# Optimization experiments

Hardware: AMD Instinct MI355X
Metric: run time of the kernel (lower is better)

Reference implementation:

```python
import jax, jax.numpy as jnp
import numpy as np

B, S, H = 16, 2048, 1024

def setup_inputs() -> dict:
    key = jax.random.key(0)
    ks = jax.random.split(key, 6)
    return {
        "h": jax.random.normal(ks[0], (1, B, H), jnp.float32),
        "c": jax.random.normal(ks[1], (1, B, H), jnp.float32),
        "encoder_outputs": jax.random.normal(ks[2], (B, S, H), jnp.float32),
        "attn_W": jax.random.normal(ks[3], (H, 2 * H), jnp.float32) * 0.02,
        "attn_b": jax.random.normal(ks[4], (H,), jnp.float32) * 0.02,
        "v_W": jax.random.normal(ks[5], (1, H), jnp.float32) * 0.02,
    }

def reference(h, c, encoder_outputs, attn_W, attn_b, v_W):
    # h: (1,B,H) -> (B,1,H); a: (B,S,H)
    a = encoder_outputs
    hq = jnp.transpose(h, (1, 0, 2))  # (B,1,H)
    # cat((s, a), -1) @ attn_W.T == s @ Wh.T + a @ Wa.T (avoids (B,S,2H) buffer)
    Wh, Wa = attn_W[:, :H], attn_W[:, H:]
    energy = jax.nn.relu(
        jnp.einsum("bqh,oh->bqo", hq, Wh)          # (B,1,H), broadcast over S
        + jnp.einsum("bsh,oh->bso", a, Wa)
        + attn_b
    )  # (B,S,H)
    scores = jnp.einsum("bsh,h->bs", energy, v_W[0])  # (B,S)
    attn_weights = jax.nn.softmax(scores, axis=1)      # (B,S)
    context = jnp.einsum("bs,bsh->bh", attn_weights, a)[:, None, :]  # (B,1,H)
    return context, attn_weights
```

## Files before the change

kernel.cpp:

```cpp
#include <hip/hip_runtime.h>
#include <hip/hip_bf16.h>


typedef __bf16 bf16x8 __attribute__((ext_vector_type(8)));
typedef float floatx4 __attribute__((ext_vector_type(4)));

#define BB 16
#define SS 2048
#define HH 1024
#define MM (BB * SS)

#define GLB(p) ((const __attribute__((address_space(1))) void*)(p))
#define LDSP(p) ((__attribute__((address_space(3))) void*)(p))

__device__ inline ushort f2bf(float x) {
    uint32_t u = __builtin_bit_cast(uint32_t, x);
    u += 0x7FFFu + ((u >> 16) & 1u);
    return (ushort)(u >> 16);
}

__global__ __launch_bounds__(256) void prep_all_kernel(
    const float* __restrict__ h, const float* __restrict__ W,
    const float* __restrict__ bias, const float* __restrict__ a,
    float* __restrict__ projh, __bf16* __restrict__ Wb, __bf16* __restrict__ Ab,
    float* __restrict__ sp0, float* __restrict__ ctx)
{
    int bid = blockIdx.x;
    int tid = threadIdx.x;
    if (bid >= 336) {
        size_t i = (size_t)(bid - 336) * 256 + tid;
        const float* s = a + i * 8;
        float4 x = *(const float4*)(s);
        float4 y = *(const float4*)(s + 4);
        union { ushort u[8]; uint4 v; } p;
        p.u[0] = f2bf(x.x); p.u[1] = f2bf(x.y); p.u[2] = f2bf(x.z); p.u[3] = f2bf(x.w);
        p.u[4] = f2bf(y.x); p.u[5] = f2bf(y.y); p.u[6] = f2bf(y.z); p.u[7] = f2bf(y.w);
        *(uint4*)(Ab + i * 8) = p.v;
    } else if (bid < 256) {
        int b = bid >> 4;
        int oc = bid & 15;
        __shared__ float hrow[HH];
        *(float4*)&hrow[tid * 4] = *(const float4*)(h + (size_t)b * HH + tid * 4);
        __syncthreads();
        int ol = tid >> 2;
        int kq = tid & 3;
        int o = oc * 64 + ol;
        const float* wr = W + (size_t)o * (2 * HH) + kq * 256;
        const float* hb = hrow + kq * 256;
        float sum = 0.f;
        for (int k = 0; k < 256; k += 4) {
            float4 wv = *(const float4*)(wr + k);
            sum += hb[k] * wv.x + hb[k + 1] * wv.y + hb[k + 2] * wv.z + hb[k + 3] * wv.w;
        }
        sum += __shfl_xor(sum, 1);
        sum += __shfl_xor(sum, 2);
        if (kq == 0) projh[b * HH + o] = sum + bias[o];
    } else if (bid < 320) {
        int cb = bid - 256;
#pragma unroll
        for (int j = 0; j < 8; j++) {
            int g = cb * 2048 + tid + j * 256;
            int o = g >> 7;
            int k = (g & 127) * 8;
            const float* s = W + (size_t)o * (2 * HH) + HH + k;
            float4 x = *(const float4*)(s);
            float4 y = *(const float4*)(s + 4);
            union { ushort u[8]; uint4 v; } p;
            p.u[0] = f2bf(x.x); p.u[1] = f2bf(x.y); p.u[2] = f2bf(x.z); p.u[3] = f2bf(x.w);
            p.u[4] = f2bf(y.x); p.u[5] = f2bf(y.y); p.u[6] = f2bf(y.z); p.u[7] = f2bf(y.w);
            *(uint4*)(Wb + (size_t)o * HH + k) = p.v;
        }
    } else {
        int zb = bid - 320;
        float4 z = make_float4(0.f, 0.f, 0.f, 0.f);
        float* sp = sp0 + zb * 2048 + tid * 8;
        *(float4*)(sp) = z;
        *(float4*)(sp + 4) = z;
        *(float4*)(ctx + zb * 1024 + tid * 4) = z;
    }
}

__global__ __launch_bounds__(512, 2) void gemm_scores_kernel(
    const __bf16* __restrict__ Ab,
    const __bf16* __restrict__ Wb,
    const float* __restrict__ projh,
    const float* __restrict__ vW,
    float* __restrict__ scores_part)
{
    __shared__ __bf16 smem[32768];

    const int bid = blockIdx.x;
    const int m0 = (((bid >> 5) << 3) + (bid & 7)) * 256;
    const int nq = (bid >> 3) & 3;
    const int n0 = nq * 256;
    const int bidx = m0 >> 11;

    const int tid = threadIdx.x;
    const int lane = tid & 63;
    const int wave = tid >> 6;
    const int wm = (wave & 1) * 128;
    const int wn = (wave >> 1) * 64;
    const int quad = lane >> 4;
    const int l16 = lane & 15;

    floatx4 acc[8][4];
    const floatx4 z = {0.f, 0.f, 0.f, 0.f};
#pragma unroll
    for (int i = 0; i < 8; i++)
#pragma unroll
        for (int j = 0; j < 4; j++) acc[i][j] = z;

    const int su = tid >> 3;
    const int sj = (tid & 7) ^ (su & 7);
    const int g_row = su * 2 + (sj >> 2);
    const int g_col = (sj & 3) * 8;
    const __bf16* gA  = Ab + (size_t)(m0 + g_row) * HH + g_col;
    const __bf16* gA2 = gA + (size_t)128 * HH;
    const __bf16* gB  = Wb + (size_t)(n0 + g_row) * HH + g_col;
    const __bf16* gB2 = gB + (size_t)128 * HH;
    const int ldsb = wave * 512;

    int aoff[8], boff[4];
#pragma unroll
    for (int i = 0; i < 8; i++) {
        int frow = wm + i * 16 + l16;
        int u2 = frow >> 1;
        int cc = u2 * 8 + (((((frow & 1) << 2) | quad)) ^ (u2 & 7));
        aoff[i] = cc * 8;
    }
#pragma unroll
    for (int j = 0; j < 4; j++) {
        int frow = wn + j * 16 + l16;
        int u2 = frow >> 1;
        int cc = u2 * 8 + (((((frow & 1) << 2) | quad)) ^ (u2 & 7));
        boff[j] = 8192 + cc * 8;
    }

#define ISSUE_STAGE(buf, k0)                                                          \
    {                                                                                 \
        __bf16* dst = smem + (buf) * 16384 + ldsb;                                    \
        __builtin_amdgcn_global_load_lds(GLB(gA  + (k0)), LDSP(dst),         16, 0, 0); \
        __builtin_amdgcn_global_load_lds(GLB(gA2 + (k0)), LDSP(dst + 4096),  16, 0, 0); \
        __builtin_amdgcn_global_load_lds(GLB(gB  + (k0)), LDSP(dst + 8192),  16, 0, 0); \
        __builtin_amdgcn_global_load_lds(GLB(gB2 + (k0)), LDSP(dst + 12288), 16, 0, 0); \
    }

    ISSUE_STAGE(0, 0)
    for (int s = 0; s < 32; s++) {
        __syncthreads();
        if (s < 31) ISSUE_STAGE((s + 1) & 1, (s + 1) * 32)
        const __bf16* sb = smem + (s & 1) * 16384;
        bf16x8 af[8], bfr[4];
#pragma unroll
        for (int j = 0; j < 4; j++) bfr[j] = *(const bf16x8*)(sb + boff[j]);
#pragma unroll
        for (int i = 0; i < 8; i++) af[i] = *(const bf16x8*)(sb + aoff[i]);
#pragma unroll
        for (int i = 0; i < 8; i++)
#pragma unroll
            for (int j = 0; j < 4; j++)
                acc[i][j] = __builtin_amdgcn_mfma_f32_16x16x32_bf16(af[i], bfr[j], acc[i][j], 0, 0, 0);
    }
#undef ISSUE_STAGE

    float ph[4], vv[4];
#pragma unroll
    for (int j = 0; j < 4; j++) {
        int ng = n0 + wn + j * 16 + l16;
        ph[j] = projh[bidx * HH + ng];
        vv[j] = vW[ng];
    }

    float* red = (float*)smem;
    if (tid < 256) red[tid] = 0.f;
    __syncthreads();

#pragma unroll
    for (int i = 0; i < 8; i++) {
        float s[4] = {0.f, 0.f, 0.f, 0.f};
#pragma unroll
        for (int j = 0; j < 4; j++) {
#pragma unroll
            for (int r2 = 0; r2 < 4; r2++) {
                float e = acc[i][j][r2] + ph[j];
                e = e > 0.f ? e : 0.f;
                s[r2] += e * vv[j];
            }
        }
#pragma unroll
        for (int r2 = 0; r2 < 4; r2++) {
            s[r2] += __shfl_xor(s[r2], 1);
            s[r2] += __shfl_xor(s[r2], 2);
            s[r2] += __shfl_xor(s[r2], 4);
            s[r2] += __shfl_xor(s[r2], 8);
        }
        if (l16 == 0) {
#pragma unroll
            for (int r2 = 0; r2 < 4; r2++)
                atomicAdd(&red[wm + i * 16 + quad * 4 + r2], s[r2]);
        }
    }
    __syncthreads();
    if (tid < 256) scores_part[(size_t)nq * MM + m0 + tid] = red[tid];
}

__global__ __launch_bounds__(256) void gemm_scores_f32_kernel(
    const float* __restrict__ A, const float* __restrict__ W,
    const float* __restrict__ projh, const float* __restrict__ vW,
    float* __restrict__ scores)
{
    constexpr int BM = 128, BN = 128, BK = 32, LDT = BK + 8;
    __shared__ __bf16 As[BM * LDT];
    __shared__ __bf16 Bs[BN * LDT];
    const int n0 = blockIdx.x * BN;
    const int m0 = blockIdx.y * BM;
    const int bidx = m0 >> 11;
    const int tid = threadIdx.x;
    const int lane = tid & 63;
    const int wave = tid >> 6;
    const int wm = (wave & 1) * 64;
    const int wn = (wave >> 1) * 64;
    const int quad = lane >> 4;
    const int l16 = lane & 15;
    floatx4 acc[4][4];
    const floatx4 z = {0.f, 0.f, 0.f, 0.f};
#pragma unroll
    for (int i = 0; i < 4; i++)
#pragma unroll
        for (int j = 0; j < 4; j++) acc[i][j] = z;
    int rowT[4], colT[4];
#pragma unroll
    for (int i = 0; i < 4; i++) {
        int fi = tid + 256 * i;
        rowT[i] = fi >> 3;
        colT[i] = (fi & 7) * 4;
    }
    for (int k0 = 0; k0 < HH; k0 += BK) {
        float4 av[4], bv[4];
#pragma unroll
        for (int i = 0; i < 4; i++) {
            av[i] = *(const float4*)(A + (size_t)(m0 + rowT[i]) * HH + k0 + colT[i]);
            bv[i] = *(const float4*)(W + (size_t)(n0 + rowT[i]) * (2 * HH) + HH + k0 + colT[i]);
        }
        __syncthreads();
#pragma unroll
        for (int i = 0; i < 4; i++) {
            ushort4 ua = make_ushort4(f2bf(av[i].x), f2bf(av[i].y), f2bf(av[i].z), f2bf(av[i].w));
            ushort4 ub = make_ushort4(f2bf(bv[i].x), f2bf(bv[i].y), f2bf(bv[i].z), f2bf(bv[i].w));
            *(ushort4*)&As[rowT[i] * LDT + colT[i]] = ua;
            *(ushort4*)&Bs[rowT[i] * LDT + colT[i]] = ub;
        }
        __syncthreads();
        bf16x8 af[4], bf[4];
#pragma unroll
        for (int i = 0; i < 4; i++)
            af[i] = *(const bf16x8*)&As[(wm + i * 16 + l16) * LDT + quad * 8];
#pragma unroll
        for (int j = 0; j < 4; j++)
            bf[j] = *(const bf16x8*)&Bs[(wn + j * 16 + l16) * LDT + quad * 8];
#pragma unroll
        for (int i = 0; i < 4; i++)
#pragma unroll
            for (int j = 0; j < 4; j++)
                acc[i][j] = __builtin_amdgcn_mfma_f32_16x16x32_bf16(af[i], bf[j], acc[i][j], 0, 0, 0);
    }
    float ph[4], vv[4];
#pragma unroll
    for (int j = 0; j < 4; j++) {
        int ng = n0 + wn + j * 16 + l16;
        ph[j] = projh[bidx * HH + ng];
        vv[j] = vW[ng];
    }
#pragma unroll
    for (int i = 0; i < 4; i++) {
        float s[4] = {0.f, 0.f, 0.f, 0.f};
#pragma unroll
        for (int j = 0; j < 4; j++) {
#pragma unroll
            for (int r = 0; r < 4; r++) {
                float e = acc[i][j][r] + ph[j];
                e = e > 0.f ? e : 0.f;
                s[r] += e * vv[j];
            }
        }
#pragma unroll
        for (int r = 0; r < 4; r++) {
            s[r] += __shfl_xor(s[r], 1);
            s[r] += __shfl_xor(s[r], 2);
            s[r] += __shfl_xor(s[r], 4);
            s[r] += __shfl_xor(s[r], 8);
        }
        if (l16 == 0) {
#pragma unroll
            for (int r = 0; r < 4; r++) {
                int mg = m0 + wm + i * 16 + quad * 4 + r;
                atomicAdd(&scores[mg], s[r]);
            }
        }
    }
}

__global__ __launch_bounds__(256) void softmax_context_kernel(
    const __bf16* __restrict__ Ab, const float* __restrict__ scores_part,
    int nparts, float* __restrict__ wout, float* __restrict__ ctx)
{
    int b = blockIdx.x >> 5;
    int sc = blockIdx.x & 31;
    int tid = threadIdx.x;
    const float* srow = scores_part + b * SS;

    float x[8];
    float mx = -1e30f;
#pragma unroll
    for (int i = 0; i < 8; i++) {
        int idx = tid + i * 256;
        float v = srow[idx];
        for (int q = 1; q < nparts; q++) v += srow[(size_t)q * MM + idx];
        x[i] = v; mx = fmaxf(mx, v);
    }
#pragma unroll
    for (int off = 32; off; off >>= 1) mx = fmaxf(mx, __shfl_xor(mx, off));
    __shared__ float redm[4], reds[4];
    if ((tid & 63) == 0) redm[tid >> 6] = mx;
    __syncthreads();
    mx = fmaxf(fmaxf(redm[0], redm[1]), fmaxf(redm[2], redm[3]));
    float sum = 0.f;
#pragma unroll
    for (int i = 0; i < 8; i++) sum += __expf(x[i] - mx);
#pragma unroll
    for (int off = 32; off; off >>= 1) sum += __shfl_xor(sum, off);
    if ((tid & 63) == 0) reds[tid >> 6] = sum;
    __syncthreads();
    float inv = 1.0f / (reds[0] + reds[1] + reds[2] + reds[3]);

    __shared__ float wsm[64];
    if (tid < 64) {
        int idx = sc * 64 + tid;
        float v = srow[idx];
        for (int q = 1; q < nparts; q++) v += srow[(size_t)q * MM + idx];
        float wv = __expf(v - mx) * inv;
        wsm[tid] = wv;
        wout[b * SS + idx] = wv;
    }
    __syncthreads();

    const __bf16* arow = Ab + ((size_t)b * SS + sc * 64) * HH + tid * 4;
    float4 acc = make_float4(0.f, 0.f, 0.f, 0.f);
#pragma unroll 4
    for (int s = 0; s < 64; s++) {
        float w = wsm[s];
        uint2 uv = *(const uint2*)(arow + (size_t)s * HH);
        float a0 = __builtin_bit_cast(float, uv.x << 16);
        float a1 = __builtin_bit_cast(float, uv.x & 0xffff0000u);
        float a2 = __builtin_bit_cast(float, uv.y << 16);
        float a3 = __builtin_bit_cast(float, uv.y & 0xffff0000u);
        acc.x += w * a0; acc.y += w * a1; acc.z += w * a2; acc.w += w * a3;
    }
    float* o = ctx + b * HH + tid * 4;
    atomicAdd(o + 0, acc.x);
    atomicAdd(o + 1, acc.y);
    atomicAdd(o + 2, acc.z);
    atomicAdd(o + 3, acc.w);
}

__global__ __launch_bounds__(256) void softmax_context_f32_kernel(
    const float* __restrict__ A, const float* __restrict__ scores_part,
    float* __restrict__ wout, float* __restrict__ ctx)
{
    int b = blockIdx.x >> 5;
    int sc = blockIdx.x & 31;
    int tid = threadIdx.x;
    const float* srow = scores_part + b * SS;
    float x[8];
    float mx = -1e30f;
#pragma unroll
    for (int i = 0; i < 8; i++) { x[i] = srow[tid + i * 256]; mx = fmaxf(mx, x[i]); }
#pragma unroll
    for (int off = 32; off; off >>= 1) mx = fmaxf(mx, __shfl_xor(mx, off));
    __shared__ float redm[4], reds[4];
    if ((tid & 63) == 0) redm[tid >> 6] = mx;
    __syncthreads();
    mx = fmaxf(fmaxf(redm[0], redm[1]), fmaxf(redm[2], redm[3]));
    float sum = 0.f;
#pragma unroll
    for (int i = 0; i < 8; i++) sum += __expf(x[i] - mx);
#pragma unroll
    for (int off = 32; off; off >>= 1) sum += __shfl_xor(sum, off);
    if ((tid & 63) == 0) reds[tid >> 6] = sum;
    __syncthreads();
    float inv = 1.0f / (reds[0] + reds[1] + reds[2] + reds[3]);
    __shared__ float wsm[64];
    if (tid < 64) {
        float wv = __expf(srow[sc * 64 + tid] - mx) * inv;
        wsm[tid] = wv;
        wout[b * SS + sc * 64 + tid] = wv;
    }
    __syncthreads();
    const float* arow = A + ((size_t)b * SS + sc * 64) * HH + tid * 4;
    float4 acc = make_float4(0.f, 0.f, 0.f, 0.f);
#pragma unroll 4
    for (int s = 0; s < 64; s++) {
        float w = wsm[s];
        float4 v = *(const float4*)(arow + (size_t)s * HH);
        acc.x += w * v.x; acc.y += w * v.y; acc.z += w * v.z; acc.w += w * v.w;
    }
    float* o = ctx + b * HH + tid * 4;
    atomicAdd(o + 0, acc.x);
    atomicAdd(o + 1, acc.y);
    atomicAdd(o + 2, acc.z);
    atomicAdd(o + 3, acc.w);
}

extern "C" void kernel_launch(void* const* d_in, const int* in_sizes, int n_in,
                              void* d_out, int out_size, void* d_ws, size_t ws_size,
                              hipStream_t stream) {
    const float* h    = (const float*)d_in[0];
    const float* a    = (const float*)d_in[2];
    const float* W    = (const float*)d_in[3];
    const float* bias = (const float*)d_in[4];
    const float* vW   = (const float*)d_in[5];
    float* out = (float*)d_out;

    float* projh       = (float*)d_ws;
    float* scores_part = projh + BB * HH;
    __bf16* Wb = (__bf16*)(scores_part + 4 * MM);
    __bf16* Ab = Wb + (size_t)HH * HH;
    const size_t need = (size_t)(BB * HH + 4 * MM) * 4 + (size_t)HH * HH * 2
                      + (size_t)MM * HH * 2;

    if (ws_size >= need) {
        prep_all_kernel<<<336 + MM * HH / 8 / 256, 256, 0, stream>>>(
            h, W, bias, a, projh, Wb, Ab, scores_part, out);
        gemm_scores_kernel<<<512, 512, 0, stream>>>(Ab, Wb, projh, vW, scores_part);
        softmax_context_kernel<<<BB * 32, 256, 0, stream>>>(
            Ab, scores_part, 4, out + BB * HH, out);
    } else {
        prep_all_kernel<<<336, 256, 0, stream>>>(h, W, bias, a, projh, Wb, Ab, scores_part, out);
        gemm_scores_f32_kernel<<<dim3(HH / 128, MM / 128), 256, 0, stream>>>(
            a, W, projh, vW, scores_part);
        softmax_context_f32_kernel<<<BB * 32, 256, 0, stream>>>(
            a, scores_part, out + BB * HH, out);
    }
}
```

Before: 299.1 us.

## Deepen GEMM LDS pipeline to four stages with split A/B loads and setprio

Replaces the double-buffered k-loop in the scores GEMM with a 4-slot LDS ring (64K bf16 of shared memory). A and B halves are staged separately and interleaved with half-tile MFMA phases, using explicit vmcnt/lgkmcnt waits, raw barriers and s_setprio around MFMA bursts. The goal is to hide global-to-LDS load latency behind more compute than the one-stage-ahead prefetch allowed. The cost is doubled LDS per block (128 KB), which may prevent the two-blocks-per-CU occupancy hinted by launch bounds. The hand-tuned wait counts and tail loads that wrap to k=0 also risk subtle synchronisation errors.

Result: faster. 292.3 us (-2.3%).

```diff
diff --git a/kernel.cpp b/kernel.cpp
--- a/kernel.cpp
+++ b/kernel.cpp
@@ -87,7 +87,7 @@
     const float* __restrict__ vW,
     float* __restrict__ scores_part)
 {
-    __shared__ __bf16 smem[32768];
+    __shared__ __bf16 smem[65536];
 
     const int bid = blockIdx.x;
     const int m0 = (((bid >> 5) << 3) + (bid & 7)) * 256;
@@ -114,54 +114,132 @@
     const int sj = (tid & 7) ^ (su & 7);
     const int g_row = su * 2 + (sj >> 2);
     const int g_col = (sj & 3) * 8;
-    const __bf16* gA  = Ab + (size_t)(m0 + g_row) * HH + g_col;
-    const __bf16* gA2 = gA + (size_t)128 * HH;
-    const __bf16* gB  = Wb + (size_t)(n0 + g_row) * HH + g_col;
-    const __bf16* gB2 = gB + (size_t)128 * HH;
-    const int ldsb = wave * 512;
+    const __bf16* gA0 = Ab + (size_t)(m0 + g_row) * HH + g_col;
+    const __bf16* gA1 = gA0 + (size_t)128 * HH;
+    const __bf16* gB0 = Wb + (size_t)(n0 + g_row) * HH + g_col;
+    const __bf16* gB1 = gB0 + (size_t)128 * HH;
+    const int wchunk = wave * 512;
 
     int aoff[8], boff[4];
 #pragma unroll
     for (int i = 0; i < 8; i++) {
         int frow = wm + i * 16 + l16;
-        int u2 = frow >> 1;
-        int cc = u2 * 8 + (((((frow & 1) << 2) | quad)) ^ (u2 & 7));
-        aoff[i] = cc * 8;
+        int r7 = frow & 127;
+        int u2 = r7 >> 1;
+        int cc = u2 * 8 + (((((r7 & 1) << 2) | quad)) ^ (u2 & 7));
+        aoff[i] = (frow >> 7) * 4096 + cc * 8;
     }
 #pragma unroll
     for (int j = 0; j < 4; j++) {
         int frow = wn + j * 16 + l16;
-        int u2 = frow >> 1;
-        int cc = u2 * 8 + (((((frow & 1) << 2) | quad)) ^ (u2 & 7));
-        boff[j] = 8192 + cc * 8;
-    }
-
-#define ISSUE_STAGE(buf, k0)                                                          \
-    {                                                                                 \
-        __bf16* dst = smem + (buf) * 16384 + ldsb;                                    \
-        __builtin_amdgcn_global_load_lds(GLB(gA  + (k0)), LDSP(dst),         16, 0, 0); \
-        __builtin_amdgcn_global_load_lds(GLB(gA2 + (k0)), LDSP(dst + 4096),  16, 0, 0); \
-        __builtin_amdgcn_global_load_lds(GLB(gB  + (k0)), LDSP(dst + 8192),  16, 0, 0); \
-        __builtin_amdgcn_global_load_lds(GLB(gB2 + (k0)), LDSP(dst + 12288), 16, 0, 0); \
-    }
-
-    ISSUE_STAGE(0, 0)
-    for (int s = 0; s < 32; s++) {
-        __syncthreads();
-        if (s < 31) ISSUE_STAGE((s + 1) & 1, (s + 1) * 32)
-        const __bf16* sb = smem + (s & 1) * 16384;
-        bf16x8 af[8], bfr[4];
-#pragma unroll
-        for (int j = 0; j < 4; j++) bfr[j] = *(const bf16x8*)(sb + boff[j]);
-#pragma unroll
-        for (int i = 0; i < 8; i++) af[i] = *(const bf16x8*)(sb + aoff[i]);
-#pragma unroll
-        for (int i = 0; i < 8; i++)
-#pragma unroll
-            for (int j = 0; j < 4; j++)
-                acc[i][j] = __builtin_amdgcn_mfma_f32_16x16x32_bf16(af[i], bfr[j], acc[i][j], 0, 0, 0);
-    }
-#undef ISSUE_STAGE
+        int r7 = frow & 127;
+        int u2 = r7 >> 1;
+        int cc = u2 * 8 + (((((r7 & 1) << 2) | quad)) ^ (u2 & 7));
+        boff[j] = 32768 + (frow >> 7) * 4096 + cc * 8;
+    }
+
+#define STAGE_A(slot, koff)                                                             \
+    {                                                                                   \
+        __bf16* d_ = smem + (slot) * 8192 + wchunk;                                     \
+        __builtin_amdgcn_global_load_lds(GLB(gA0 + (koff)), LDSP(d_), 16, 0, 0);        \
+        __builtin_amdgcn_global_load_lds(GLB(gA1 + (koff)), LDSP(d_ + 4096), 16, 0, 0); \
+    }
+#define STAGE_B(slot, koff)                                                             \
+    {                                                                                   \
+        __bf16* d_ = smem + 32768 + (slot) * 8192 + wchunk;                             \
+        __builtin_amdgcn_global_load_lds(GLB(gB0 + (koff)), LDSP(d_), 16, 0, 0);        \
+        __builtin_amdgcn_global_load_lds(GLB(gB1 + (koff)), LDSP(d_ + 4096), 16, 0, 0); \
+    }
+#define READ_BFR(base)                                     \
+    {                                                      \
+        bfr[0] = *(const bf16x8*)((base) + boff[0]);       \
+        bfr[1] = *(const bf16x8*)((base) + boff[1]);       \
+        bfr[2] = *(const bf16x8*)((base) + boff[2]);       \
+        bfr[3] = *(const bf16x8*)((base) + boff[3]);       \
+    }
+#define READ_ALO(base)                                     \
+    {                                                      \
+        af[0] = *(const bf16x8*)((base) + aoff[0]);        \
+        af[1] = *(const bf16x8*)((base) + aoff[1]);        \
+        af[2] = *(const bf16x8*)((base) + aoff[2]);        \
+        af[3] = *(const bf16x8*)((base) + aoff[3]);        \
+    }
+#define READ_AHI(base)                                     \
+    {                                                      \
+        af2[0] = *(const bf16x8*)((base) + aoff[4]);       \
+        af2[1] = *(const bf16x8*)((base) + aoff[5]);       \
+        af2[2] = *(const bf16x8*)((base) + aoff[6]);       \
+        af2[3] = *(const bf16x8*)((base) + aoff[7]);       \
+    }
+#define MFMA_LO                                                                            \
+    _Pragma("unroll") for (int i_ = 0; i_ < 4; i_++)                                       \
+        _Pragma("unroll") for (int j_ = 0; j_ < 4; j_++)                                   \
+            acc[i_][j_] = __builtin_amdgcn_mfma_f32_16x16x32_bf16(af[i_], bfr[j_], acc[i_][j_], 0, 0, 0);
+#define MFMA_HI                                                                            \
+    _Pragma("unroll") for (int i_ = 0; i_ < 4; i_++)                                       \
+        _Pragma("unroll") for (int j_ = 0; j_ < 4; j_++)                                   \
+            acc[i_ + 4][j_] = __builtin_amdgcn_mfma_f32_16x16x32_bf16(af2[i_], bfr[j_], acc[i_ + 4][j_], 0, 0, 0);
+#define BAR __builtin_amdgcn_s_barrier()
+#define LGKM0 asm volatile("s_waitcnt lgkmcnt(0)" ::: "memory")
+#define VM8 asm volatile("s_waitcnt vmcnt(8)" ::: "memory")
+#define PRIO1 __builtin_amdgcn_s_setprio(1)
+#define PRIO0 __builtin_amdgcn_s_setprio(0)
+
+#define SPAN(P, K1, K2)                              \
+    {                                                \
+        const __bf16* cb0 = smem + (P) * 16384;      \
+        const __bf16* cb1 = cb0 + 8192;              \
+                                        \
+        READ_BFR(cb0); READ_ALO(cb0);                \
+        STAGE_A((1 - (P)) * 2 + 1, K1);              \
+        BAR; LGKM0; PRIO1; MFMA_LO; PRIO0; BAR;      \
+                                        \
+        READ_AHI(cb0);                               \
+        STAGE_B((1 - (P)) * 2 + 1, K1);              \
+        VM8;                                         \
+        BAR; LGKM0; PRIO1; MFMA_HI; PRIO0; BAR;      \
+                                        \
+        READ_BFR(cb1); READ_ALO(cb1);                \
+        STAGE_A((P) * 2, K2);                        \
+        BAR; LGKM0; PRIO1; MFMA_LO; PRIO0; BAR;      \
+                                        \
+        READ_AHI(cb1);                               \
+        STAGE_B((P) * 2, K2);                        \
+        VM8;                                         \
+        BAR; LGKM0; PRIO1; MFMA_HI; PRIO0; BAR;      \
+    }
+
+    bf16x8 af[4], af2[4], bfr[4];
+
+    STAGE_A(0, 0);  STAGE_B(0, 0);
+    STAGE_A(1, 32); STAGE_B(1, 32);
+    STAGE_A(2, 64); STAGE_B(2, 64);
+    VM8;
+    BAR;
+
+    for (int it = 0; it < 8; ++it) {
+        const int kb = it * 128;
+        const int k1 = kb + 96;
+        const int k2 = (it < 7) ? kb + 128 : 0;
+        const int k3 = (it < 7) ? kb + 160 : 0;
+        const int k4 = (it < 7) ? kb + 192 : 0;
+        SPAN(0, k1, k2)
+        SPAN(1, k3, k4)
+    }
+
+#undef SPAN
+#undef STAGE_A
+#undef STAGE_B
+#undef READ_BFR
+#undef READ_ALO
+#undef READ_AHI
+#undef MFMA_LO
+#undef MFMA_HI
+#undef BAR
+#undef LGKM0
+#undef VM8
+#undef PRIO1
+#undef PRIO0
 
     float ph[4], vv[4];
 #pragma unroll
```

## Fuse fp32-to-bf16 conversion of encoder outputs into GEMM LDS pipeline

Applied to the files above, without the earlier changes.

Drops the separate pass that converted encoder outputs to bf16. The GEMM kernel now streams fp32 A tiles into LDS with a triple-buffered async pipeline and converts them to bf16 in registers before the MFMAs, with barriers, waitcnts and priority hints. The context kernel reads fp32 encoder outputs directly. This removes a full-tensor read/write pass, but the GEMM and context reads double in bytes and the larger LDS footprint lowers occupancy.

After: 288.0 us. -3.7%, faster.

```diff
diff --git a/kernel.cpp b/kernel.cpp
--- a/kernel.cpp
+++ b/kernel.cpp
@@ -21,22 +21,13 @@
 
 __global__ __launch_bounds__(256) void prep_all_kernel(
     const float* __restrict__ h, const float* __restrict__ W,
-    const float* __restrict__ bias, const float* __restrict__ a,
-    float* __restrict__ projh, __bf16* __restrict__ Wb, __bf16* __restrict__ Ab,
+    const float* __restrict__ bias,
+    float* __restrict__ projh, __bf16* __restrict__ Wb,
     float* __restrict__ sp0, float* __restrict__ ctx)
 {
     int bid = blockIdx.x;
     int tid = threadIdx.x;
-    if (bid >= 336) {
-        size_t i = (size_t)(bid - 336) * 256 + tid;
-        const float* s = a + i * 8;
-        float4 x = *(const float4*)(s);
-        float4 y = *(const float4*)(s + 4);
-        union { ushort u[8]; uint4 v; } p;
-        p.u[0] = f2bf(x.x); p.u[1] = f2bf(x.y); p.u[2] = f2bf(x.z); p.u[3] = f2bf(x.w);
-        p.u[4] = f2bf(y.x); p.u[5] = f2bf(y.y); p.u[6] = f2bf(y.z); p.u[7] = f2bf(y.w);
-        *(uint4*)(Ab + i * 8) = p.v;
-    } else if (bid < 256) {
+    if (bid < 256) {
         int b = bid >> 4;
         int oc = bid & 15;
         __shared__ float hrow[HH];
@@ -81,13 +72,14 @@
 }
 
 __global__ __launch_bounds__(512, 2) void gemm_scores_kernel(
-    const __bf16* __restrict__ Ab,
+    const float* __restrict__ Af,
     const __bf16* __restrict__ Wb,
     const float* __restrict__ projh,
     const float* __restrict__ vW,
     float* __restrict__ scores_part)
 {
-    __shared__ __bf16 smem[32768];
+    __shared__ __align__(16) char smem_raw[147456];
+    __bf16* sB = (__bf16*)(smem_raw + 98304);
 
     const int bid = blockIdx.x;
     const int m0 = (((bid >> 5) << 3) + (bid & 7)) * 256;
@@ -110,58 +102,143 @@
 #pragma unroll
         for (int j = 0; j < 4; j++) acc[i][j] = z;
 
+    const int rb = lane >> 3;
+    const int cchunk = ((lane & 7) ^ rb) * 4;
+    const float* gAq0 = Af + (size_t)(m0 +   0 + wave * 8 + rb) * HH + cchunk;
+    const float* gAq1 = Af + (size_t)(m0 +  64 + wave * 8 + rb) * HH + cchunk;
+    const float* gAq2 = Af + (size_t)(m0 + 128 + wave * 8 + rb) * HH + cchunk;
+    const float* gAq3 = Af + (size_t)(m0 + 192 + wave * 8 + rb) * HH + cchunk;
+
     const int su = tid >> 3;
     const int sj = (tid & 7) ^ (su & 7);
     const int g_row = su * 2 + (sj >> 2);
     const int g_col = (sj & 3) * 8;
-    const __bf16* gA  = Ab + (size_t)(m0 + g_row) * HH + g_col;
-    const __bf16* gA2 = gA + (size_t)128 * HH;
-    const __bf16* gB  = Wb + (size_t)(n0 + g_row) * HH + g_col;
-    const __bf16* gB2 = gB + (size_t)128 * HH;
-    const int ldsb = wave * 512;
-
-    int aoff[8], boff[4];
-#pragma unroll
-    for (int i = 0; i < 8; i++) {
-        int frow = wm + i * 16 + l16;
-        int u2 = frow >> 1;
-        int cc = u2 * 8 + (((((frow & 1) << 2) | quad)) ^ (u2 & 7));
-        aoff[i] = cc * 8;
-    }
+    const __bf16* gB0 = Wb + (size_t)(n0 + g_row) * HH + g_col;
+    const __bf16* gB1 = gB0 + (size_t)128 * HH;
+
+    const int axL = (quad * 32) ^ ((l16 & 7) << 4);
+    const int axH = axL ^ 16;
+    int arow[8];
+#pragma unroll
+    for (int i = 0; i < 8; i++) arow[i] = (wm + i * 16 + l16) * 128;
+
+    int boff[4];
 #pragma unroll
     for (int j = 0; j < 4; j++) {
         int frow = wn + j * 16 + l16;
-        int u2 = frow >> 1;
-        int cc = u2 * 8 + (((((frow & 1) << 2) | quad)) ^ (u2 & 7));
-        boff[j] = 8192 + cc * 8;
-    }
-
-#define ISSUE_STAGE(buf, k0)                                                          \
-    {                                                                                 \
-        __bf16* dst = smem + (buf) * 16384 + ldsb;                                    \
-        __builtin_amdgcn_global_load_lds(GLB(gA  + (k0)), LDSP(dst),         16, 0, 0); \
-        __builtin_amdgcn_global_load_lds(GLB(gA2 + (k0)), LDSP(dst + 4096),  16, 0, 0); \
-        __builtin_amdgcn_global_load_lds(GLB(gB  + (k0)), LDSP(dst + 8192),  16, 0, 0); \
-        __builtin_amdgcn_global_load_lds(GLB(gB2 + (k0)), LDSP(dst + 12288), 16, 0, 0); \
-    }
-
-    ISSUE_STAGE(0, 0)
-    for (int s = 0; s < 32; s++) {
-        __syncthreads();
-        if (s < 31) ISSUE_STAGE((s + 1) & 1, (s + 1) * 32)
-        const __bf16* sb = smem + (s & 1) * 16384;
-        bf16x8 af[8], bfr[4];
-#pragma unroll
-        for (int j = 0; j < 4; j++) bfr[j] = *(const bf16x8*)(sb + boff[j]);
-#pragma unroll
-        for (int i = 0; i < 8; i++) af[i] = *(const bf16x8*)(sb + aoff[i]);
-#pragma unroll
-        for (int i = 0; i < 8; i++)
-#pragma unroll
-            for (int j = 0; j < 4; j++)
-                acc[i][j] = __builtin_amdgcn_mfma_f32_16x16x32_bf16(af[i], bfr[j], acc[i][j], 0, 0, 0);
-    }
-#undef ISSUE_STAGE
+        int r7 = frow & 127;
+        int u2 = r7 >> 1;
+        int cc = u2 * 8 + (((((r7 & 1) << 2) | quad)) ^ (u2 & 7));
+        boff[j] = (frow >> 7) * 4096 + cc * 8;
+    }
+
+#define STAGE_A(S, KF)                                                                       \
+    {                                                                                        \
+        char* dA_ = smem_raw + (S) * 32768 + wave * 1024;                                    \
+        __builtin_amdgcn_global_load_lds(GLB(gAq0 + (KF)), LDSP(dA_), 16, 0, 0);             \
+        __builtin_amdgcn_global_load_lds(GLB(gAq1 + (KF)), LDSP(dA_ + 8192), 16, 0, 0);      \
+        __builtin_amdgcn_global_load_lds(GLB(gAq2 + (KF)), LDSP(dA_ + 16384), 16, 0, 0);     \
+        __builtin_amdgcn_global_load_lds(GLB(gAq3 + (KF)), LDSP(dA_ + 24576), 16, 0, 0);     \
+    }
+#define STAGE_B(S, KF)                                                                       \
+    {                                                                                        \
+        __bf16* dB_ = sB + (S) * 8192 + wave * 512;                                          \
+        __builtin_amdgcn_global_load_lds(GLB(gB0 + (KF)), LDSP(dB_), 16, 0, 0);              \
+        __builtin_amdgcn_global_load_lds(GLB(gB1 + (KF)), LDSP(dB_ + 4096), 16, 0, 0);       \
+    }
+#define CVT8(dst, L, H)                                                     \
+    {                                                                       \
+        dst[0] = (__bf16)(L).x; dst[1] = (__bf16)(L).y;                     \
+        dst[2] = (__bf16)(L).z; dst[3] = (__bf16)(L).w;                     \
+        dst[4] = (__bf16)(H).x; dst[5] = (__bf16)(H).y;                     \
+        dst[6] = (__bf16)(H).z; dst[7] = (__bf16)(H).w;                     \
+    }
+#define MFMA_LO                                                                            \
+    _Pragma("unroll") for (int i_ = 0; i_ < 4; i_++)                                       \
+        _Pragma("unroll") for (int j_ = 0; j_ < 4; j_++)                                   \
+            acc[i_][j_] = __builtin_amdgcn_mfma_f32_16x16x32_bf16(af[i_], bfr[j_], acc[i_][j_], 0, 0, 0);
+#define MFMA_HI                                                                            \
+    _Pragma("unroll") for (int i_ = 0; i_ < 4; i_++)                                       \
+        _Pragma("unroll") for (int j_ = 0; j_ < 4; j_++)                                   \
+            acc[i_ + 4][j_] = __builtin_amdgcn_mfma_f32_16x16x32_bf16(af2[i_], bfr[j_], acc[i_ + 4][j_], 0, 0, 0);
+#define BAR __builtin_amdgcn_s_barrier()
+#define LGKM0 asm volatile("s_waitcnt lgkmcnt(0)" ::: "memory")
+#define VM6 asm volatile("s_waitcnt vmcnt(6)" ::: "memory")
+#define VM0 asm volatile("s_waitcnt vmcnt(0)" ::: "memory")
+#define NOPW
+#define PRIO1 __builtin_amdgcn_s_setprio(1)
+#define PRIO0 __builtin_amdgcn_s_setprio(0)
+
+#define KTILE(SC, SN, KF, DOST, VMW_)                                        \
+    {                                                                        \
+        const char* ab_ = smem_raw + (SC) * 32768;                           \
+        const __bf16* bb_ = sB + (SC) * 8192;                                \
+                                                                \
+        bfr[0] = *(const bf16x8*)(bb_ + boff[0]);                            \
+        bfr[1] = *(const bf16x8*)(bb_ + boff[1]);                            \
+        bfr[2] = *(const bf16x8*)(bb_ + boff[2]);                            \
+        bfr[3] = *(const bf16x8*)(bb_ + boff[3]);                            \
+        floatx4 aL0 = *(const floatx4*)(ab_ + arow[0] + axL);                \
+        floatx4 aH0 = *(const floatx4*)(ab_ + arow[0] + axH);                \
+        floatx4 aL1 = *(const floatx4*)(ab_ + arow[1] + axL);                \
+        floatx4 aH1 = *(const floatx4*)(ab_ + arow[1] + axH);                \
+        floatx4 aL2 = *(const floatx4*)(ab_ + arow[2] + axL);                \
+        floatx4 aH2 = *(const floatx4*)(ab_ + arow[2] + axH);                \
+        floatx4 aL3 = *(const floatx4*)(ab_ + arow[3] + axL);                \
+        floatx4 aH3 = *(const floatx4*)(ab_ + arow[3] + axH);                \
+        if (DOST) STAGE_A(SN, KF);                                           \
+        BAR; LGKM0;                                                          \
+        CVT8(af[0], aL0, aH0); CVT8(af[1], aL1, aH1);                        \
+        CVT8(af[2], aL2, aH2); CVT8(af[3], aL3, aH3);                        \
+        PRIO1; MFMA_LO; PRIO0; BAR;                                          \
+                                                                \
+        floatx4 cL0 = *(const floatx4*)(ab_ + arow[4] + axL);                \
+        floatx4 cH0 = *(const floatx4*)(ab_ + arow[4] + axH);                \
+        floatx4 cL1 = *(const floatx4*)(ab_ + arow[5] + axL);                \
+        floatx4 cH1 = *(const floatx4*)(ab_ + arow[5] + axH);                \
+        floatx4 cL2 = *(const floatx4*)(ab_ + arow[6] + axL);                \
+        floatx4 cH2 = *(const floatx4*)(ab_ + arow[6] + axH);                \
+        floatx4 cL3 = *(const floatx4*)(ab_ + arow[7] + axL);                \
+        floatx4 cH3 = *(const floatx4*)(ab_ + arow[7] + axH);                \
+        if (DOST) STAGE_B(SN, KF);                                           \
+        VMW_;                                                                \
+        BAR; LGKM0;                                                          \
+        CVT8(af2[0], cL0, cH0); CVT8(af2[1], cL1, cH1);                      \
+        CVT8(af2[2], cL2, cH2); CVT8(af2[3], cL3, cH3);                      \
+        PRIO1; MFMA_HI; PRIO0; BAR;                                          \
+    }
+
+    bf16x8 af[4], af2[4], bfr[4];
+
+    STAGE_A(0, 0);
+    STAGE_B(0, 0);
+    STAGE_A(1, 32);
+    STAGE_B(1, 32);
+    VM6;
+    BAR;
+
+    for (int g = 0; g < 10; ++g) {
+        const int kf0 = (3 * g + 2) * 32;
+        KTILE(0, 2, kf0, 1, VM6)
+        KTILE(1, 0, kf0 + 32, 1, VM6)
+        KTILE(2, 1, kf0 + 64, 1, VM6)
+    }
+    KTILE(0, 2, 0, 0, VM0)
+    KTILE(1, 0, 0, 0, NOPW)
+
+#undef KTILE
+#undef STAGE_A
+#undef STAGE_B
+#undef CVT8
+#undef MFMA_LO
+#undef MFMA_HI
+#undef BAR
+#undef LGKM0
+#undef VM6
+#undef VM0
+#undef NOPW
+#undef PRIO1
+#undef PRIO0
 
     float ph[4], vv[4];
 #pragma unroll
@@ -171,7 +248,8 @@
         vv[j] = vW[ng];
     }
 
-    float* red = (float*)smem;
+    float* red = (float*)smem_raw;
+    __syncthreads();
     if (tid < 256) red[tid] = 0.f;
     __syncthreads();
 
@@ -301,7 +379,7 @@
 }
 
 __global__ __launch_bounds__(256) void softmax_context_kernel(
-    const __bf16* __restrict__ Ab, const float* __restrict__ scores_part,
+    const float* __restrict__ A, const float* __restrict__ scores_part,
     int nparts, float* __restrict__ wout, float* __restrict__ ctx)
 {
     int b = blockIdx.x >> 5;
@@ -344,58 +422,6 @@
     }
     __syncthreads();
 
-    const __bf16* arow = Ab + ((size_t)b * SS + sc * 64) * HH + tid * 4;
-    float4 acc = make_float4(0.f, 0.f, 0.f, 0.f);
-#pragma unroll 4
-    for (int s = 0; s < 64; s++) {
-        float w = wsm[s];
-        uint2 uv = *(const uint2*)(arow + (size_t)s * HH);
-        float a0 = __builtin_bit_cast(float, uv.x << 16);
-        float a1 = __builtin_bit_cast(float, uv.x & 0xffff0000u);
-        float a2 = __builtin_bit_cast(float, uv.y << 16);
-        float a3 = __builtin_bit_cast(float, uv.y & 0xffff0000u);
-        acc.x += w * a0; acc.y += w * a1; acc.z += w * a2; acc.w += w * a3;
-    }
-    float* o = ctx + b * HH + tid * 4;
-    atomicAdd(o + 0, acc.x);
-    atomicAdd(o + 1, acc.y);
-    atomicAdd(o + 2, acc.z);
-    atomicAdd(o + 3, acc.w);
-}
-
-__global__ __launch_bounds__(256) void softmax_context_f32_kernel(
-    const float* __restrict__ A, const float* __restrict__ scores_part,
-    float* __restrict__ wout, float* __restrict__ ctx)
-{
-    int b = blockIdx.x >> 5;
-    int sc = blockIdx.x & 31;
-    int tid = threadIdx.x;
-    const float* srow = scores_part + b * SS;
-    float x[8];
-    float mx = -1e30f;
-#pragma unroll
-    for (int i = 0; i < 8; i++) { x[i] = srow[tid + i * 256]; mx = fmaxf(mx, x[i]); }
-#pragma unroll
-    for (int off = 32; off; off >>= 1) mx = fmaxf(mx, __shfl_xor(mx, off));
-    __shared__ float redm[4], reds[4];
-    if ((tid & 63) == 0) redm[tid >> 6] = mx;
-    __syncthreads();
-    mx = fmaxf(fmaxf(redm[0], redm[1]), fmaxf(redm[2], redm[3]));
-    float sum = 0.f;
-#pragma unroll
-    for (int i = 0; i < 8; i++) sum += __expf(x[i] - mx);
-#pragma unroll
-    for (int off = 32; off; off >>= 1) sum += __shfl_xor(sum, off);
-    if ((tid & 63) == 0) reds[tid >> 6] = sum;
-    __syncthreads();
-    float inv = 1.0f / (reds[0] + reds[1] + reds[2] + reds[3]);
-    __shared__ float wsm[64];
-    if (tid < 64) {
-        float wv = __expf(srow[sc * 64 + tid] - mx) * inv;
-        wsm[tid] = wv;
-        wout[b * SS + sc * 64 + tid] = wv;
-    }
-    __syncthreads();
     const float* arow = A + ((size_t)b * SS + sc * 64) * HH + tid * 4;
     float4 acc = make_float4(0.f, 0.f, 0.f, 0.f);
 #pragma unroll 4
@@ -424,21 +450,18 @@
     float* projh       = (float*)d_ws;
     float* scores_part = projh + BB * HH;
     __bf16* Wb = (__bf16*)(scores_part + 4 * MM);
-    __bf16* Ab = Wb + (size_t)HH * HH;
-    const size_t need = (size_t)(BB * HH + 4 * MM) * 4 + (size_t)HH * HH * 2
-                      + (size_t)MM * HH * 2;
+    const size_t need = (size_t)(BB * HH + 4 * MM) * 4 + (size_t)HH * HH * 2;
 
     if (ws_size >= need) {
-        prep_all_kernel<<<336 + MM * HH / 8 / 256, 256, 0, stream>>>(
-            h, W, bias, a, projh, Wb, Ab, scores_part, out);
-        gemm_scores_kernel<<<512, 512, 0, stream>>>(Ab, Wb, projh, vW, scores_part);
+        prep_all_kernel<<<336, 256, 0, stream>>>(h, W, bias, projh, Wb, scores_part, out);
+        gemm_scores_kernel<<<512, 512, 0, stream>>>(a, Wb, projh, vW, scores_part);
         softmax_context_kernel<<<BB * 32, 256, 0, stream>>>(
-            Ab, scores_part, 4, out + BB * HH, out);
+            a, scores_part, 4, out + BB * HH, out);
     } else {
-        prep_all_kernel<<<336, 256, 0, stream>>>(h, W, bias, a, projh, Wb, Ab, scores_part, out);
+        prep_all_kernel<<<336, 256, 0, stream>>>(h, W, bias, projh, Wb, scores_part, out);
         gemm_scores_f32_kernel<<<dim3(HH / 128, MM / 128), 256, 0, stream>>>(
             a, W, projh, vW, scores_part);
-        softmax_context_f32_kernel<<<BB * 32, 256, 0, stream>>>(
-            a, scores_part, out + BB * HH, out);
-    }
-}
+        softmax_context_kernel<<<BB * 32, 256, 0, stream>>>(
+            a, scores_part, 1, out + BB * HH, out);
+    }
+}
```

## Triple-buffer A tiles with explicit vmcnt waits and MFMA priority hints

Applied to the files above, without the earlier changes.

Restructures the GEMM main loop from a double-buffered single-barrier pipeline into a 3-stage A / 2-stage B pipeline, unrolled by six per group. It waits with explicit s_waitcnt vmcnt counts and a raw s_barrier instead of a full __syncthreads each step. The MFMA block is split in two halves with s_setprio raised around them to favour matrix issue. LDS use grows from 64KB to 80KB per block, which may conflict with the two-blocks-per-CU launch bound, and the hand-placed wait counts are easy to get wrong.

New measurement: 293.3 us. Within noise of the previous version (-1.9%).

```diff
diff --git a/kernel.cpp b/kernel.cpp
--- a/kernel.cpp
+++ b/kernel.cpp
@@ -87,7 +87,7 @@
     const float* __restrict__ vW,
     float* __restrict__ scores_part)
 {
-    __shared__ __bf16 smem[32768];
+    __shared__ __bf16 smem[40960];
 
     const int bid = blockIdx.x;
     const int m0 = (((bid >> 5) << 3) + (bid & 7)) * 256;
@@ -114,54 +114,114 @@
     const int sj = (tid & 7) ^ (su & 7);
     const int g_row = su * 2 + (sj >> 2);
     const int g_col = (sj & 3) * 8;
-    const __bf16* gA  = Ab + (size_t)(m0 + g_row) * HH + g_col;
-    const __bf16* gA2 = gA + (size_t)128 * HH;
-    const __bf16* gB  = Wb + (size_t)(n0 + g_row) * HH + g_col;
-    const __bf16* gB2 = gB + (size_t)128 * HH;
-    const int ldsb = wave * 512;
+    const __bf16* gA0 = Ab + (size_t)(m0 + g_row) * HH + g_col;
+    const __bf16* gA1 = gA0 + (size_t)128 * HH;
+    const __bf16* gB0 = Wb + (size_t)(n0 + g_row) * HH + g_col;
+    const __bf16* gB1 = gB0 + (size_t)128 * HH;
+    const int wchunk = wave * 512;
 
     int aoff[8], boff[4];
 #pragma unroll
     for (int i = 0; i < 8; i++) {
         int frow = wm + i * 16 + l16;
-        int u2 = frow >> 1;
-        int cc = u2 * 8 + (((((frow & 1) << 2) | quad)) ^ (u2 & 7));
-        aoff[i] = cc * 8;
+        int r7 = frow & 127;
+        int u2 = r7 >> 1;
+        int cc = u2 * 8 + (((((r7 & 1) << 2) | quad)) ^ (u2 & 7));
+        aoff[i] = (frow >> 7) * 4096 + cc * 8;
     }
 #pragma unroll
     for (int j = 0; j < 4; j++) {
         int frow = wn + j * 16 + l16;
-        int u2 = frow >> 1;
-        int cc = u2 * 8 + (((((frow & 1) << 2) | quad)) ^ (u2 & 7));
-        boff[j] = 8192 + cc * 8;
-    }
-
-#define ISSUE_STAGE(buf, k0)                                                          \
-    {                                                                                 \
-        __bf16* dst = smem + (buf) * 16384 + ldsb;                                    \
-        __builtin_amdgcn_global_load_lds(GLB(gA  + (k0)), LDSP(dst),         16, 0, 0); \
-        __builtin_amdgcn_global_load_lds(GLB(gA2 + (k0)), LDSP(dst + 4096),  16, 0, 0); \
-        __builtin_amdgcn_global_load_lds(GLB(gB  + (k0)), LDSP(dst + 8192),  16, 0, 0); \
-        __builtin_amdgcn_global_load_lds(GLB(gB2 + (k0)), LDSP(dst + 12288), 16, 0, 0); \
-    }
-
-    ISSUE_STAGE(0, 0)
-    for (int s = 0; s < 32; s++) {
-        __syncthreads();
-        if (s < 31) ISSUE_STAGE((s + 1) & 1, (s + 1) * 32)
-        const __bf16* sb = smem + (s & 1) * 16384;
-        bf16x8 af[8], bfr[4];
-#pragma unroll
-        for (int j = 0; j < 4; j++) bfr[j] = *(const bf16x8*)(sb + boff[j]);
-#pragma unroll
-        for (int i = 0; i < 8; i++) af[i] = *(const bf16x8*)(sb + aoff[i]);
-#pragma unroll
-        for (int i = 0; i < 8; i++)
-#pragma unroll
-            for (int j = 0; j < 4; j++)
-                acc[i][j] = __builtin_amdgcn_mfma_f32_16x16x32_bf16(af[i], bfr[j], acc[i][j], 0, 0, 0);
-    }
-#undef ISSUE_STAGE
+        int r7 = frow & 127;
+        int u2 = r7 >> 1;
+        int cc = u2 * 8 + (((((r7 & 1) << 2) | quad)) ^ (u2 & 7));
+        boff[j] = (frow >> 7) * 4096 + cc * 8;
+    }
+
+#define STAGE_A(S, KF)                                                                  \
+    {                                                                                   \
+        __bf16* d_ = smem + (S) * 8192 + wchunk;                                        \
+        __builtin_amdgcn_global_load_lds(GLB(gA0 + (KF)), LDSP(d_), 16, 0, 0);          \
+        __builtin_amdgcn_global_load_lds(GLB(gA1 + (KF)), LDSP(d_ + 4096), 16, 0, 0);   \
+    }
+#define STAGE_B(S, KF)                                                                  \
+    {                                                                                   \
+        __bf16* d_ = smem + 24576 + (S) * 8192 + wchunk;                                \
+        __builtin_amdgcn_global_load_lds(GLB(gB0 + (KF)), LDSP(d_), 16, 0, 0);          \
+        __builtin_amdgcn_global_load_lds(GLB(gB1 + (KF)), LDSP(d_ + 4096), 16, 0, 0);   \
+    }
+#define BAR __builtin_amdgcn_s_barrier()
+#define VM2 asm volatile("s_waitcnt vmcnt(2)" ::: "memory")
+#define VM0 asm volatile("s_waitcnt vmcnt(0)" ::: "memory")
+#define PRIO1 __builtin_amdgcn_s_setprio(1)
+#define PRIO0 __builtin_amdgcn_s_setprio(0)
+
+#define COMPUTE(AS, BS)                                                      \
+    {                                                                        \
+        const __bf16* ab_ = smem + (AS) * 8192;                              \
+        const __bf16* bb_ = smem + 24576 + (BS) * 8192;                      \
+        bf16x8 af[4], af2[4], bfr[4];                                        \
+        bfr[0] = *(const bf16x8*)(bb_ + boff[0]);                            \
+        bfr[1] = *(const bf16x8*)(bb_ + boff[1]);                            \
+        bfr[2] = *(const bf16x8*)(bb_ + boff[2]);                            \
+        bfr[3] = *(const bf16x8*)(bb_ + boff[3]);                            \
+        af[0] = *(const bf16x8*)(ab_ + aoff[0]);                             \
+        af[1] = *(const bf16x8*)(ab_ + aoff[1]);                             \
+        af[2] = *(const bf16x8*)(ab_ + aoff[2]);                             \
+        af[3] = *(const bf16x8*)(ab_ + aoff[3]);                             \
+        PRIO1;                                                               \
+        _Pragma("unroll") for (int i_ = 0; i_ < 4; i_++)                     \
+            _Pragma("unroll") for (int j_ = 0; j_ < 4; j_++)                 \
+                acc[i_][j_] = __builtin_amdgcn_mfma_f32_16x16x32_bf16(       \
+                    af[i_], bfr[j_], acc[i_][j_], 0, 0, 0);                  \
+        PRIO0;                                                               \
+        af2[0] = *(const bf16x8*)(ab_ + aoff[4]);                            \
+        af2[1] = *(const bf16x8*)(ab_ + aoff[5]);                            \
+        af2[2] = *(const bf16x8*)(ab_ + aoff[6]);                            \
+        af2[3] = *(const bf16x8*)(ab_ + aoff[7]);                            \
+        PRIO1;                                                               \
+        _Pragma("unroll") for (int i_ = 0; i_ < 4; i_++)                     \
+            _Pragma("unroll") for (int j_ = 0; j_ < 4; j_++)                 \
+                acc[i_ + 4][j_] = __builtin_amdgcn_mfma_f32_16x16x32_bf16(   \
+                    af2[i_], bfr[j_], acc[i_ + 4][j_], 0, 0, 0);             \
+        PRIO0;                                                               \
+    }
+
+#define KT(U)                                                                \
+    {                                                                        \
+        STAGE_B((U + 1) % 2, k6 + (U + 1) * 32);                             \
+        STAGE_A((U + 2) % 3, k6 + (U + 2) * 32);                             \
+        COMPUTE(U % 3, U % 2)                                                \
+        VM2;                                                                 \
+        BAR;                                                                 \
+    }
+
+    STAGE_A(0, 0);
+    STAGE_B(0, 0);
+    STAGE_A(1, 32);
+    VM2;
+    BAR;
+
+    for (int g = 0; g < 5; ++g) {
+        const int k6 = g * 192;
+        KT(0) KT(1) KT(2) KT(3) KT(4) KT(5)
+    }
+
+    STAGE_B(1, 992);
+    COMPUTE(0, 0)
+    VM0;
+    BAR;
+    COMPUTE(1, 1)
+
+#undef KT
+#undef COMPUTE
+#undef STAGE_A
+#undef STAGE_B
+#undef BAR
+#undef VM2
+#undef VM0
+#undef PRIO1
+#undef PRIO0
 
     float ph[4], vv[4];
 #pragma unroll
@@ -172,6 +232,7 @@
     }
 
     float* red = (float*)smem;
+    __syncthreads();
     if (tid < 256) red[tid] = 0.f;
     __syncthreads();
 
```
